# Kernel tuning notes

Hardware: AMD Instinct MI355X
Metric: run time of the kernel (lower is better)

## Reference

```python
import jax, jax.numpy as jnp
import numpy as np

D_MODEL = 4096
D_FIBER = 64
D_LATENT = 512
OMEGA = 0.1
B, L = 4, 4096


def cayley(A):
    # Q = (I - A)^{-1} (I + A), batched over leading dim; A is skew-symmetric
    d = A.shape[-1]
    I = jnp.eye(d, dtype=A.dtype)
    return jnp.linalg.solve(I - A, I + A)


def setup_inputs() -> dict:
    key = jax.random.key(0)
    k1, k2, k3, k4, k5 = jax.random.split(key, 5)
    h_t = jax.random.normal(k1, (B, L, D_MODEL), dtype=jnp.float32)
    z0 = jax.random.normal(k2, (B, D_LATENT), dtype=jnp.float32)
    A_raw = jax.random.normal(k3, (B, D_FIBER, D_FIBER), dtype=jnp.float32) * 0.1
    A_u = A_raw - jnp.swapaxes(A_raw, -1, -2)  # skew-symmetric gauge connection
    # frozen projection weights, torch nn.Linear layout: (out_features, in_features)
    W_down = jax.random.normal(k4, (D_FIBER, D_MODEL), dtype=jnp.float32) / np.sqrt(D_MODEL)
    W_up = jax.random.normal(k5, (D_MODEL, D_FIBER), dtype=jnp.float32) / np.sqrt(D_FIBER)
    alpha = jnp.float32(OMEGA)
    return {"h_t": h_t, "z0": z0, "A_u": A_u, "alpha": alpha, "W_down": W_down, "W_up": W_up}


def reference(h_t, z0, A_u, alpha, W_down, W_up):
    # psi_down: (B,L,d_model) @ (d_model,d_fiber)
    h_fiber = jnp.einsum('bld,fd->blf', h_t, W_down)
    Q_u = cayley(A_u)  # (B, d_fiber, d_fiber)
    # h_fiber @ Q_u^T per batch
    h_rot = jnp.einsum('blf,bgf->blg', h_fiber, Q_u)
    delta = h_rot - h_fiber
    h_out = h_t + alpha * jnp.einsum('blf,df->bld', delta, W_up)
    return h_out
```

## Files before the change

kernel.cpp:

```cpp
#include <hip/hip_runtime.h>
#include <hip/hip_bf16.h>

#define D_MODEL 4096
#define NFIB    64
#define NBATCH  4
#define LSEQ    4096
#define TM      16
#define TILES   (LSEQ / TM)
#define KC      512
#define NKC     (D_MODEL / KC)

typedef __attribute__((ext_vector_type(4))) float f32x4;
typedef __attribute__((ext_vector_type(8))) short bf16x8;

__device__ __forceinline__ unsigned short f2bf(float f) {
  unsigned int u = __builtin_bit_cast(unsigned int, f);
  u += 0x7FFFu + ((u >> 16) & 1u);
  return (unsigned short)(u >> 16);
}

__global__ __launch_bounds__(256) void cayley_kernel(const float* __restrict__ A,
                                                     float* __restrict__ S) {
  __shared__ float M[64][66];
  __shared__ float R[64][66];
  const int b = blockIdx.x;
  const int tid = threadIdx.x;
  const int k = tid & 63;
  const int g = tid >> 6;
  const float* Ab = A + b * 4096;
#pragma unroll
  for (int ii = 0; ii < 16; ++ii) {
    int i = g * 16 + ii;
    float a = Ab[i * 64 + k];
    M[i][k] = ((i == k) ? 1.0f : 0.0f) - a;
    R[i][k] = 2.0f * a;
  }
  __syncthreads();
  for (int j = 0; j < 64; ++j) {
    float inv = 1.0f / M[j][j];
    __syncthreads();
    if (g == 0) { M[j][k] *= inv; R[j][k] *= inv; }
    __syncthreads();
    float mjk = M[j][k], rjk = R[j][k];
    float f[16];
#pragma unroll
    for (int ii = 0; ii < 16; ++ii) f[ii] = M[g * 16 + ii][j];
    __syncthreads();
#pragma unroll
    for (int ii = 0; ii < 16; ++ii) {
      int i = g * 16 + ii;
      if (i != j) {
        M[i][k] -= f[ii] * mjk;
        R[i][k] -= f[ii] * rjk;
      }
    }
    __syncthreads();
  }
  float* Sb = S + b * 4096;
#pragma unroll
  for (int ii = 0; ii < 16; ++ii) {
    int i = g * 16 + ii;
    Sb[i * 64 + k] = R[i][k];
  }
}

__global__ void cvt_wd_kernel(const float* __restrict__ Wd, unsigned short* __restrict__ Wd2) {
  int idx = blockIdx.x * 256 + threadIdx.x;
  int j    = idx & 7;
  int lane = (idx >> 3) & 63;
  int nf   = (idx >> 9) & 3;
  int ks   = idx >> 11;
  int row = nf * 16 + (lane & 15);
  int col = ks * 32 + (lane >> 4) * 8 + j;
  Wd2[idx] = f2bf(Wd[row * D_MODEL + col]);
}

__global__ void prep_u_kernel(const float* __restrict__ Wup, const float* __restrict__ S,
                              const float* __restrict__ alpha_p,
                              unsigned short* __restrict__ U2) {
  int idx = blockIdx.x * 256 + threadIdx.x;
  int j    = idx & 7;
  int h    = (idx >> 3) & 1;
  int lane = (idx >> 4) & 63;
  int nt   = (idx >> 10) & 255;
  int b    = idx >> 18;
  int d = nt * 16 + (lane & 15);
  int f = h * 32 + (lane >> 4) * 8 + j;
  const float* Sb = S + b * 4096;
  const float alpha = alpha_p[0];
  float s = 0.f;
#pragma unroll 8
  for (int g = 0; g < 64; ++g) s += Wup[d * 64 + g] * Sb[g * 64 + f];
  U2[idx] = f2bf(alpha * s);
}

__global__ __launch_bounds__(256) void main_kernel(
    const float* __restrict__ H, const unsigned short* __restrict__ Wd2,
    const unsigned short* __restrict__ U2, float* __restrict__ Out) {
  const int blk = blockIdx.x;
  const int b = blk >> 8;
  const int t = blk & 255;
  const int row0 = b * LSEQ + t * TM;

  const int tid = threadIdx.x;
  const int w = tid >> 6, l = tid & 63, lr = l & 15, lq = l >> 4;

  __shared__ unsigned short Hs[TM * KC];
  __shared__ __attribute__((aligned(16))) unsigned short Fb[TM][72];

  const int srow  = w;
  const int scolb = l * 16;

  const float* hbase = H + (size_t)row0 * D_MODEL;
  char* hsb = (char*)Hs;

  int wb[4];
#pragma unroll
  for (int j = 0; j < 4; ++j) {
    int row = 4 * j + srow;
    wb[j] = row * 1024 + (scolb ^ ((row & 7) << 4));
  }

  f32x4 cur[8];
#pragma unroll
  for (int j = 0; j < 4; ++j) {
    const float* p = hbase + (size_t)(4 * j + srow) * D_MODEL + l * 8;
    cur[2 * j]     = *(const f32x4*)p;
    cur[2 * j + 1] = *(const f32x4*)(p + 4);
  }

  f32x4 acc = {0, 0, 0, 0};
  const unsigned short* wdbase = Wd2 + w * 512 + l * 8;

  for (int kc = 0; kc < NKC; ++kc) {
    asm volatile("s_waitcnt lgkmcnt(0)" ::: "memory");
    __builtin_amdgcn_s_barrier();

#pragma unroll
    for (int j = 0; j < 4; ++j) {
      f32x4 a0 = cur[2 * j], a1 = cur[2 * j + 1];
      bf16x8 v;
      v[0] = (short)f2bf(a0[0]); v[1] = (short)f2bf(a0[1]);
      v[2] = (short)f2bf(a0[2]); v[3] = (short)f2bf(a0[3]);
      v[4] = (short)f2bf(a1[0]); v[5] = (short)f2bf(a1[1]);
      v[6] = (short)f2bf(a1[2]); v[7] = (short)f2bf(a1[3]);
      *(bf16x8*)(hsb + wb[j]) = v;
    }

    f32x4 nxt[8];
    if (kc < NKC - 1) {
#pragma unroll
      for (int j = 0; j < 4; ++j) {
        const float* p = hbase + (size_t)(4 * j + srow) * D_MODEL + (kc + 1) * KC + l * 8;
        nxt[2 * j]     = *(const f32x4*)p;
        nxt[2 * j + 1] = *(const f32x4*)(p + 4);
      }
    }

    asm volatile("s_waitcnt lgkmcnt(0)" ::: "memory");
    __builtin_amdgcn_s_barrier();

    const unsigned short* wp = wdbase + (size_t)kc * 16 * 2048;
#pragma unroll
    for (int s = 0; s < 16; ++s) {
      bf16x8 afr = *(const bf16x8*)(hsb + lr * 1024 + ((s * 64 + lq * 16) ^ ((lr & 7) << 4)));
      bf16x8 bfr = *(const bf16x8*)(wp + (size_t)s * 2048);
      acc = __builtin_amdgcn_mfma_f32_16x16x32_bf16(afr, bfr, acc, 0, 0, 0);
    }

    if (kc < NKC - 1) {
#pragma unroll
      for (int q = 0; q < 8; ++q) cur[q] = nxt[q];
    }
  }

  Fb[lq * 4 + 0][w * 16 + lr] = f2bf(acc[0]);
  Fb[lq * 4 + 1][w * 16 + lr] = f2bf(acc[1]);
  Fb[lq * 4 + 2][w * 16 + lr] = f2bf(acc[2]);
  Fb[lq * 4 + 3][w * 16 + lr] = f2bf(acc[3]);
  __syncthreads();

  bf16x8 fa0 = *(const bf16x8*)(&Fb[lr][lq * 8]);
  bf16x8 fa1 = *(const bf16x8*)(&Fb[lr][32 + lq * 8]);

  const unsigned short* ub = U2 + (((size_t)(b * 256) + w * 64) * 64 + l) * 16;
  const int nbase = w * 1024;
#pragma unroll 4
  for (int nf = 0; nf < 64; ++nf) {
    const unsigned short* up = ub + (size_t)nf * 1024;
    bf16x8 u0 = *(const bf16x8*)(up);
    bf16x8 u1 = *(const bf16x8*)(up + 8);
    f32x4 c = {0, 0, 0, 0};
    c = __builtin_amdgcn_mfma_f32_16x16x32_bf16(fa0, u0, c, 0, 0, 0);
    c = __builtin_amdgcn_mfma_f32_16x16x32_bf16(fa1, u1, c, 0, 0, 0);
    const int n = nbase + nf * 16;
#pragma unroll
    for (int rr = 0; rr < 4; ++rr) {
      size_t o = (size_t)(row0 + lq * 4 + rr) * D_MODEL + n + lr;
      Out[o] = H[o] + c[rr];
    }
  }
}

extern "C" void kernel_launch(void* const* d_in, const int* in_sizes, int n_in,
                              void* d_out, int out_size, void* d_ws, size_t ws_size,
                              hipStream_t stream) {
  const float* h_t    = (const float*)d_in[0];
  const float* A_u    = (const float*)d_in[2];
  const float* alpha  = (const float*)d_in[3];
  const float* W_down = (const float*)d_in[4];
  const float* W_up   = (const float*)d_in[5];
  float* out = (float*)d_out;

  char* ws = (char*)d_ws;
  float*          S   = (float*)ws;
  unsigned short* Wd2 = (unsigned short*)(ws + 65536);
  unsigned short* U2  = (unsigned short*)(ws + 65536 + 524288);

  cayley_kernel<<<NBATCH, 256, 0, stream>>>(A_u, S);
  cvt_wd_kernel<<<(NFIB * D_MODEL) / 256, 256, 0, stream>>>(W_down, Wd2);
  prep_u_kernel<<<(NBATCH * D_MODEL * NFIB) / 256, 256, 0, stream>>>(W_up, S, alpha, U2);
  main_kernel<<<NBATCH * TILES, 256, 0, stream>>>(h_t, Wd2, U2, out);
}
```

Baseline: 307.5 us.

## Load H fragments straight from global into MFMA operands, dropping the LDS staging

The down-projection loop in the main kernel no longer stages the H tile through shared memory behind barriers. Each wave now loads its 16x32 slice of H from global memory every step, converts it to bf16 with packed intrinsics and feeds it straight into the MFMA. This removes the LDS writes, the barriers and the software double-buffering, at the cost of all four waves reading the same H tile, so global/L1 traffic and conversion work rise fourfold. prep_u_kernel also caches the Cayley matrix in LDS and reads W_up with vector loads, and main_kernel gets an occupancy hint of 4 blocks per CU in its launch bounds.

```diff
diff --git a/kernel.cpp b/kernel.cpp
--- a/kernel.cpp
+++ b/kernel.cpp
@@ -7,8 +7,6 @@
 #define LSEQ    4096
 #define TM      16
 #define TILES   (LSEQ / TM)
-#define KC      512
-#define NKC     (D_MODEL / KC)
 
 typedef __attribute__((ext_vector_type(4))) float f32x4;
 typedef __attribute__((ext_vector_type(8))) short bf16x8;
@@ -17,6 +15,15 @@
   unsigned int u = __builtin_bit_cast(unsigned int, f);
   u += 0x7FFFu + ((u >> 16) & 1u);
   return (unsigned short)(u >> 16);
+}
+
+__device__ __forceinline__ bf16x8 cvt8(f32x4 a, f32x4 b) {
+  union { __hip_bfloat162 h2[4]; bf16x8 v; } u;
+  u.h2[0] = __float22bfloat162_rn(make_float2(a[0], a[1]));
+  u.h2[1] = __float22bfloat162_rn(make_float2(a[2], a[3]));
+  u.h2[2] = __float22bfloat162_rn(make_float2(b[0], b[1]));
+  u.h2[3] = __float22bfloat162_rn(make_float2(b[2], b[3]));
+  return u.v;
 }
 
 __global__ __launch_bounds__(256) void cayley_kernel(const float* __restrict__ A,
@@ -75,26 +82,38 @@
   Wd2[idx] = f2bf(Wd[row * D_MODEL + col]);
 }
 
-__global__ void prep_u_kernel(const float* __restrict__ Wup, const float* __restrict__ S,
-                              const float* __restrict__ alpha_p,
-                              unsigned short* __restrict__ U2) {
-  int idx = blockIdx.x * 256 + threadIdx.x;
-  int j    = idx & 7;
-  int h    = (idx >> 3) & 1;
-  int lane = (idx >> 4) & 63;
-  int nt   = (idx >> 10) & 255;
-  int b    = idx >> 18;
-  int d = nt * 16 + (lane & 15);
-  int f = h * 32 + (lane >> 4) * 8 + j;
+__global__ __launch_bounds__(256) void prep_u_kernel(const float* __restrict__ Wup,
+                                                     const float* __restrict__ S,
+                                                     const float* __restrict__ alpha_p,
+                                                     unsigned short* __restrict__ U2) {
+  __shared__ float Sl[4096];
+  const int idx0 = blockIdx.x * 256;
+  const int b = idx0 >> 18;
   const float* Sb = S + b * 4096;
+  for (int i = threadIdx.x; i < 1024; i += 256)
+    ((f32x4*)Sl)[i] = ((const f32x4*)Sb)[i];
+  __syncthreads();
+
+  const int idx = idx0 + threadIdx.x;
+  const int j    = idx & 7;
+  const int h    = (idx >> 3) & 1;
+  const int lane = (idx >> 4) & 63;
+  const int nt   = (idx >> 10) & 255;
+  const int d = nt * 16 + (lane & 15);
+  const int f = h * 32 + (lane >> 4) * 8 + j;
   const float alpha = alpha_p[0];
+  const f32x4* wr = (const f32x4*)(Wup + d * 64);
   float s = 0.f;
-#pragma unroll 8
-  for (int g = 0; g < 64; ++g) s += Wup[d * 64 + g] * Sb[g * 64 + f];
+#pragma unroll
+  for (int g4 = 0; g4 < 16; ++g4) {
+    f32x4 wv = wr[g4];
+    s += wv[0] * Sl[(g4 * 4 + 0) * 64 + f] + wv[1] * Sl[(g4 * 4 + 1) * 64 + f] +
+         wv[2] * Sl[(g4 * 4 + 2) * 64 + f] + wv[3] * Sl[(g4 * 4 + 3) * 64 + f];
+  }
   U2[idx] = f2bf(alpha * s);
 }
 
-__global__ __launch_bounds__(256) void main_kernel(
+__global__ __launch_bounds__(256, 4) void main_kernel(
     const float* __restrict__ H, const unsigned short* __restrict__ Wd2,
     const unsigned short* __restrict__ U2, float* __restrict__ Out) {
   const int blk = blockIdx.x;
@@ -105,73 +124,19 @@
   const int tid = threadIdx.x;
   const int w = tid >> 6, l = tid & 63, lr = l & 15, lq = l >> 4;
 
-  __shared__ unsigned short Hs[TM * KC];
   __shared__ __attribute__((aligned(16))) unsigned short Fb[TM][72];
 
-  const int srow  = w;
-  const int scolb = l * 16;
-
-  const float* hbase = H + (size_t)row0 * D_MODEL;
-  char* hsb = (char*)Hs;
-
-  int wb[4];
-#pragma unroll
-  for (int j = 0; j < 4; ++j) {
-    int row = 4 * j + srow;
-    wb[j] = row * 1024 + (scolb ^ ((row & 7) << 4));
-  }
-
-  f32x4 cur[8];
-#pragma unroll
-  for (int j = 0; j < 4; ++j) {
-    const float* p = hbase + (size_t)(4 * j + srow) * D_MODEL + l * 8;
-    cur[2 * j]     = *(const f32x4*)p;
-    cur[2 * j + 1] = *(const f32x4*)(p + 4);
-  }
+  const float* ha = H + (size_t)(row0 + lr) * D_MODEL + lq * 8;
+  const unsigned short* wb = Wd2 + w * 512 + l * 8;
 
   f32x4 acc = {0, 0, 0, 0};
-  const unsigned short* wdbase = Wd2 + w * 512 + l * 8;
-
-  for (int kc = 0; kc < NKC; ++kc) {
-    asm volatile("s_waitcnt lgkmcnt(0)" ::: "memory");
-    __builtin_amdgcn_s_barrier();
-
-#pragma unroll
-    for (int j = 0; j < 4; ++j) {
-      f32x4 a0 = cur[2 * j], a1 = cur[2 * j + 1];
-      bf16x8 v;
-      v[0] = (short)f2bf(a0[0]); v[1] = (short)f2bf(a0[1]);
-      v[2] = (short)f2bf(a0[2]); v[3] = (short)f2bf(a0[3]);
-      v[4] = (short)f2bf(a1[0]); v[5] = (short)f2bf(a1[1]);
-      v[6] = (short)f2bf(a1[2]); v[7] = (short)f2bf(a1[3]);
-      *(bf16x8*)(hsb + wb[j]) = v;
-    }
-
-    f32x4 nxt[8];
-    if (kc < NKC - 1) {
-#pragma unroll
-      for (int j = 0; j < 4; ++j) {
-        const float* p = hbase + (size_t)(4 * j + srow) * D_MODEL + (kc + 1) * KC + l * 8;
-        nxt[2 * j]     = *(const f32x4*)p;
-        nxt[2 * j + 1] = *(const f32x4*)(p + 4);
-      }
-    }
-
-    asm volatile("s_waitcnt lgkmcnt(0)" ::: "memory");
-    __builtin_amdgcn_s_barrier();
-
-    const unsigned short* wp = wdbase + (size_t)kc * 16 * 2048;
-#pragma unroll
-    for (int s = 0; s < 16; ++s) {
-      bf16x8 afr = *(const bf16x8*)(hsb + lr * 1024 + ((s * 64 + lq * 16) ^ ((lr & 7) << 4)));
-      bf16x8 bfr = *(const bf16x8*)(wp + (size_t)s * 2048);
-      acc = __builtin_amdgcn_mfma_f32_16x16x32_bf16(afr, bfr, acc, 0, 0, 0);
-    }
-
-    if (kc < NKC - 1) {
-#pragma unroll
-      for (int q = 0; q < 8; ++q) cur[q] = nxt[q];
-    }
+#pragma unroll 4
+  for (int s = 0; s < 128; ++s) {
+    f32x4 h0 = *(const f32x4*)(ha + s * 32);
+    f32x4 h1 = *(const f32x4*)(ha + s * 32 + 4);
+    bf16x8 bfr = *(const bf16x8*)(wb + (size_t)s * 2048);
+    bf16x8 afr = cvt8(h0, h1);
+    acc = __builtin_amdgcn_mfma_f32_16x16x32_bf16(afr, bfr, acc, 0, 0, 0);
   }
 
   Fb[lq * 4 + 0][w * 16 + lr] = f2bf(acc[0]);
```

After: 482.3 us. +56.8%, slower.
